# Performance work log

Hardware: AMD Instinct MI355X
Metric: run time of the kernel (lower is better)

The kernel has to match this reference:

```python
import jax, jax.numpy as jnp
import numpy as np
from jax import lax

BLANK = 27
NEG = -1e30  # safe -inf substitute (avoids NaN grads through logaddexp)


def _joint_log_probs(enc, dec, We, Wd, bf, Wp, bp):
    # Concat-then-Linear == sum of per-branch matmuls: [e;d] @ Wf = e@We + d@Wd.
    f = jnp.einsum('bte,eh->bth', enc, We)          # [B,T,H]
    g = jnp.einsum('bud,dh->buh', dec, Wd)          # [B,U1,H]
    h = jnp.tanh(f[:, :, None, :] + g[:, None, :, :] + bf)  # [B,T,U1,H]
    logits = jnp.einsum('btuh,hv->btuv', h, Wp) + bp         # [B,T,U1,V]
    return jax.nn.log_softmax(logits, axis=-1)


def _rnnt_loss_one(lp, tgt, t_len, u_len):
    # lp: [T,U1,V] log-probs, tgt: [U] int labels, t_len/u_len: scalars.
    T, U1, V = lp.shape
    blank_lp = lp[:, :, BLANK]                                   # [T,U1]
    lab_lp = jnp.take_along_axis(lp[:, :U1 - 1, :],
                                 tgt[None, :, None], axis=2)[..., 0]  # [T,U]

    # alpha[0,:] : only label emissions along u at t=0.
    alpha0 = jnp.concatenate([jnp.zeros((1,), lp.dtype),
                              jnp.cumsum(lab_lp[0])])            # [U1]

    def step(prev_alpha, inp):
        b_prev, lab_t = inp                       # [U1], [U]
        from_below = prev_alpha + b_prev          # blank move from t-1
        first = from_below[0]

        def inner(carry, x):
            fb, lab = x
            new = jnp.logaddexp(fb, carry + lab)  # blank-from-below vs label-from-left
            return new, new

        _, rest = lax.scan(inner, first, (from_below[1:], lab_t))
        alpha_t = jnp.concatenate([first[None], rest])
        return alpha_t, alpha_t

    _, alphas = lax.scan(step, alpha0, (blank_lp[:-1], lab_lp[1:]))
    alpha = jnp.concatenate([alpha0[None], alphas], axis=0)      # [T,U1]

    # Terminal: emit final blank at (t_len-1, u_len).
    return -(alpha[t_len - 1, u_len] + blank_lp[t_len - 1, u_len])


def setup_inputs() -> dict:
    key = jax.random.key(0)
    ks = jax.random.split(key, 10)
    B, T, U, E, D, H, V = 8, 400, 60, 256, 256, 512, 28
    enc_state = jax.random.normal(ks[0], (B, T, E), jnp.float32)
    dec_state = jax.random.normal(ks[1], (B, U + 1, D), jnp.float32)
    targets = jax.random.randint(ks[2], (B, U), 0, BLANK, jnp.int32)
    inputs_length = jax.random.randint(ks[3], (B,), 200, T + 1, jnp.int32)
    targets_length = jax.random.randint(ks[4], (B,), 30, U + 1, jnp.int32)
    s1 = 1.0 / np.sqrt(E + D)
    s2 = 1.0 / np.sqrt(H)
    We = jax.random.normal(ks[5], (E, H), jnp.float32) * s1
    Wd = jax.random.normal(ks[6], (D, H), jnp.float32) * s1
    bf = jax.random.normal(ks[7], (H,), jnp.float32) * s1
    Wp = jax.random.normal(ks[8], (H, V), jnp.float32) * s2
    bp = jax.random.normal(ks[9], (V,), jnp.float32) * s2
    return {"enc_state": enc_state, "dec_state": dec_state,
            "We": We, "Wd": Wd, "bf": bf, "Wp": Wp, "bp": bp,
            "targets": targets, "inputs_length": inputs_length,
            "targets_length": targets_length}


def reference(enc_state, dec_state, We, Wd, bf, Wp, bp,
              targets, inputs_length, targets_length):
    lp = _joint_log_probs(enc_state, dec_state, We, Wd, bf, Wp, bp)
    loss = jax.vmap(_rnnt_loss_one)(lp, targets, inputs_length, targets_length)
    return loss  # [B], reduction='none'
```

## Files before the change

### kernel.cpp

```cpp
#include <hip/hip_runtime.h>
#include <hip/hip_bf16.h>
#include <math.h>

#define NEGF (-1e30f)
#define LOG2E 1.4426950408889634f

typedef __attribute__((ext_vector_type(8))) short bf16x8;
typedef __attribute__((ext_vector_type(4))) float f32x4;

#define DROWS_PAD 480
#define DPITCH 64
#define D_TRIP 464
#define PF 16

__device__ __forceinline__ float tanh_fast(float x) {
    float e2 = __builtin_amdgcn_exp2f(x * 2.885390081777927f);
    return fmaf(-2.f, __builtin_amdgcn_rcpf(e2 + 1.f), 1.f);
}

__device__ __forceinline__ unsigned short f2bf(float x) {
    __hip_bfloat16 h = __float2bfloat16(x);
    return *reinterpret_cast<unsigned short*>(&h);
}

__device__ __forceinline__ float wave_shr1(float x) {
    int i = __builtin_bit_cast(int, x);
    int r = __builtin_amdgcn_update_dpp(0, i, 0x138, 0xf, 0xf, true);
    return __builtin_bit_cast(float, r);
}

__global__ __launch_bounds__(256) void k_pack(const float* __restrict__ We,
                                              const float* __restrict__ Wd,
                                              const float* __restrict__ Wp,
                                              unsigned short* __restrict__ WeFrag,
                                              unsigned short* __restrict__ WdFrag,
                                              unsigned short* __restrict__ BfragP) {
    int gid = blockIdx.x * 256 + threadIdx.x;
    if (gid < 32768) {
        const float* W = (gid < 16384) ? We : Wd;
        unsigned short* F = (gid < 16384) ? WeFrag : WdFrag;
        int s = gid & 16383;
        int lane = s & 63;
        int c = (s >> 6) & 7;
        int nt = s >> 9;
        int n = nt * 16 + (lane & 15);
        int kbase = c * 32 + ((lane >> 4) & 3) * 8;
        unsigned short* dst = F + (size_t)s * 8;
#pragma unroll
        for (int j = 0; j < 8; ++j) dst[j] = f2bf(W[(size_t)(kbase + j) * 512 + n]);
    } else if (gid < 34816) {
        int s = gid - 32768;
        int lane = s & 63;
        int half = (s >> 6) & 1;
        int c = s >> 7;
        int n = half * 16 + (lane & 15);
        int kbase = c * 32 + (lane >> 4) * 8;
        unsigned short* dst = BfragP + (size_t)s * 8;
#pragma unroll
        for (int j = 0; j < 8; ++j) {
            float v = (n < 28) ? Wp[(kbase + j) * 28 + n] : 0.f;
            dst[j] = f2bf(v);
        }
    }
}

__global__ __launch_bounds__(256) void k_gemm(const float* __restrict__ enc,
                                              const float* __restrict__ dec,
                                              const float* __restrict__ bfv,
                                              const unsigned short* __restrict__ WeFrag,
                                              const unsigned short* __restrict__ WdFrag,
                                              float* __restrict__ f,
                                              float* __restrict__ g) {
    const int wid = blockIdx.x * 4 + threadIdx.y;
    const int lane = threadIdx.x;
    const int m16 = lane & 15;
    const int quad = lane >> 4;

    const float* A; const unsigned short* WF; float* Out; int M, rt, ct; bool isg;
    if (wid < 1600) { A = enc; WF = WeFrag; Out = f; M = 3200; rt = wid >> 3; ct = wid & 7; isg = false; }
    else { int w2 = wid - 1600; A = dec; WF = WdFrag; Out = g; M = 488; rt = w2 >> 3; ct = w2 & 7; isg = true; }

    const int row = rt * 16 + m16;
    const float* arow = A + (size_t)min(row, M - 1) * 256 + quad * 8;

    f32x4 acc[4];
#pragma unroll
    for (int i = 0; i < 4; ++i) acc[i] = (f32x4){0.f, 0.f, 0.f, 0.f};

#pragma unroll
    for (int c = 0; c < 8; ++c) {
        float4 a0 = *(const float4*)(arow + c * 32);
        float4 a1 = *(const float4*)(arow + c * 32 + 4);
        union { unsigned short s[8]; bf16x8 v; } Af;
        Af.s[0] = f2bf(a0.x); Af.s[1] = f2bf(a0.y);
        Af.s[2] = f2bf(a0.z); Af.s[3] = f2bf(a0.w);
        Af.s[4] = f2bf(a1.x); Af.s[5] = f2bf(a1.y);
        Af.s[6] = f2bf(a1.z); Af.s[7] = f2bf(a1.w);
#pragma unroll
        for (int i = 0; i < 4; ++i) {
            int nt = ct * 4 + i;
            bf16x8 Bv = *(const bf16x8*)(WF + (size_t)((nt * 8 + c) * 64 + lane) * 8);
            acc[i] = __builtin_amdgcn_mfma_f32_16x16x32_bf16(Af.v, Bv, acc[i], 0, 0, 0);
        }
    }

#pragma unroll
    for (int i = 0; i < 4; ++i) {
        int n = ct * 64 + i * 16 + m16;
        float bv = isg ? bfv[n] : 0.f;
#pragma unroll
        for (int r = 0; r < 4; ++r) {
            int ro = rt * 16 + quad * 4 + r;
            if (ro < M) Out[(size_t)ro * 512 + n] = acc[i][r] + bv;
        }
    }
}

__global__ __launch_bounds__(256) void k_cells(const float* __restrict__ f,
                                               const float* __restrict__ g,
                                               const unsigned short* __restrict__ Bfrag,
                                               const float* __restrict__ bp,
                                               const int* __restrict__ targets,
                                               const int* __restrict__ ilen,
                                               float2* __restrict__ pairD) {
    const int b = blockIdx.z;
    const int tlen = ilen[b];
    const int t0 = blockIdx.x * 16;
    if (t0 >= tlen) return;
    const int wave = threadIdx.y;
    const int lane = threadIdx.x;
    const int u_raw = blockIdx.y * 4 + wave;
    const int u = min(u_raw, 60);
    const int tid = wave * 64 + lane;

    __shared__ float fs[16 * 516];

    {
        const float4* src = (const float4*)(f + (size_t)(b * 400 + t0) * 512);
#pragma unroll
        for (int i = 0; i < 8; ++i) {
            int idx = tid + i * 256;
            int row = idx >> 7;
            int c4 = idx & 127;
            float4 v = src[idx];
            *(float4*)&fs[row * 516 + c4 * 4] = v;
        }
    }
    __syncthreads();

    const int quad = lane >> 4;
    const int m16 = lane & 15;
    const float* gu = g + (size_t)(b * 61 + u) * 512 + quad * 8;
    const float* fsrow = fs + m16 * 516 + quad * 8;
    f32x4 acc0 = {0.f, 0.f, 0.f, 0.f};
    f32x4 acc1 = {0.f, 0.f, 0.f, 0.f};

#pragma unroll 4
    for (int c = 0; c < 16; ++c) {
        float4 fa = *(const float4*)(fsrow + c * 32);
        float4 fb = *(const float4*)(fsrow + c * 32 + 4);
        float4 ga = *(const float4*)(gu + c * 32);
        float4 gb = *(const float4*)(gu + c * 32 + 4);
        union { unsigned short s[8]; bf16x8 v; } A;
        A.s[0] = f2bf(tanh_fast(fa.x + ga.x));
        A.s[1] = f2bf(tanh_fast(fa.y + ga.y));
        A.s[2] = f2bf(tanh_fast(fa.z + ga.z));
        A.s[3] = f2bf(tanh_fast(fa.w + ga.w));
        A.s[4] = f2bf(tanh_fast(fb.x + gb.x));
        A.s[5] = f2bf(tanh_fast(fb.y + gb.y));
        A.s[6] = f2bf(tanh_fast(fb.z + gb.z));
        A.s[7] = f2bf(tanh_fast(fb.w + gb.w));
        bf16x8 B0 = *(const bf16x8*)(Bfrag + ((size_t)(c * 2 + 0) * 64 + lane) * 8);
        bf16x8 B1 = *(const bf16x8*)(Bfrag + ((size_t)(c * 2 + 1) * 64 + lane) * 8);
        acc0 = __builtin_amdgcn_mfma_f32_16x16x32_bf16(A.v, B0, acc0, 0, 0, 0);
        acc1 = __builtin_amdgcn_mfma_f32_16x16x32_bf16(A.v, B1, acc1, 0, 0, 0);
    }

    float bp0 = bp[m16];
    int n1 = 16 + m16;
    bool n1v = (n1 < 28);
    float bp1 = n1v ? bp[n1] : 0.f;
    int tv = targets[b * 60 + min(u, 59)];

    float res_blank[4], res_lab[4];
#pragma unroll
    for (int r = 0; r < 4; ++r) {
        float l0 = acc0[r] + bp0;
        float l1 = n1v ? (acc1[r] + bp1) : NEGF;
        float mx = fmaxf(l0, l1);
        mx = fmaxf(mx, __shfl_xor(mx, 1, 64));
        mx = fmaxf(mx, __shfl_xor(mx, 2, 64));
        mx = fmaxf(mx, __shfl_xor(mx, 4, 64));
        mx = fmaxf(mx, __shfl_xor(mx, 8, 64));
        float s = __builtin_amdgcn_exp2f((l0 - mx) * LOG2E) +
                  __builtin_amdgcn_exp2f((l1 - mx) * LOG2E);
        s += __shfl_xor(s, 1, 64);
        s += __shfl_xor(s, 2, 64);
        s += __shfl_xor(s, 4, 64);
        s += __shfl_xor(s, 8, 64);
        float lse = mx + __logf(s);
        int base = lane & 48;
        float labsrc = (tv < 16) ? l0 : l1;
        float labv = __shfl(labsrc, base | (tv & 15), 64);
        float blankv = __shfl(l1, base | 11, 64);
        res_blank[r] = blankv - lse;
        res_lab[r] = labv - lse;
    }

    if (m16 == 0 && u_raw <= 60) {
        float2* Pd = pairD + (size_t)b * (DROWS_PAD * DPITCH);
#pragma unroll
        for (int r = 0; r < 4; ++r) {
            int t = t0 + quad * 4 + r;
            if (t < tlen) {
                int d = t + u;
                float2 pr;
                pr.x = res_blank[r];
                pr.y = (u <= 59) ? res_lab[r] : NEGF;
                Pd[d * DPITCH + u] = pr;
            }
        }
    }
}

__global__ __launch_bounds__(64) void k_alpha(const float2* __restrict__ pairD,
                                              const int* __restrict__ ilen,
                                              const int* __restrict__ ulenp,
                                              float* __restrict__ out) {
    const int b = blockIdx.x;
    const int u = threadIdx.x;
    const float2* Pd = pairD + (size_t)b * (DROWS_PAD * DPITCH);
    const int tl = ilen[b];
    const int ul = ulenp[b];
    const int dstar = tl - 1 + ul;
    const bool uok = (u <= 60);
    const bool lok = (u >= 1 && u <= 60);

    float cur = (u == 0) ? 0.f : NEGF;
    float saved = NEGF;

    float2 pf[PF];
#pragma unroll
    for (int i = 0; i < PF; ++i) pf[i] = Pd[i * DPITCH + u];

    for (int d0 = 1; d0 <= D_TRIP; d0 += PF) {
#pragma unroll
        for (int i = 0; i < PF; ++i) {
            const int d = d0 + i;
            float2 v = pf[i];
            pf[i] = Pd[(d + PF - 1) * DPITCH + u];
            int t = d - u;
            float bv = (t >= 1 && t <= 399 && uok) ? v.x : NEGF;
            float lvn = wave_shr1(v.y);
            float lv = (lok && t >= 0 && t <= 399) ? lvn : NEGF;
            float up = wave_shr1(cur);
            float a = cur + bv;
            float c2 = up + lv;
            float mx = fmaxf(a, c2), mn = fminf(a, c2);
            float nv = mx + __logf(1.f + __builtin_amdgcn_exp2f((mn - mx) * LOG2E));
            bool valid = (t >= 0 && t <= 399 && uok);
            cur = valid ? nv : cur;
            saved = (d == dstar) ? cur : saved;
        }
    }
    if (u == ul) out[b] = -(saved + Pd[dstar * DPITCH + u].x);
}

extern "C" void kernel_launch(void* const* d_in, const int* in_sizes, int n_in,
                              void* d_out, int out_size, void* d_ws, size_t ws_size,
                              hipStream_t stream) {
    const float* enc = (const float*)d_in[0];
    const float* dec = (const float*)d_in[1];
    const float* We  = (const float*)d_in[2];
    const float* Wd  = (const float*)d_in[3];
    const float* bf  = (const float*)d_in[4];
    const float* Wp  = (const float*)d_in[5];
    const float* bp  = (const float*)d_in[6];
    const int* targets = (const int*)d_in[7];
    const int* ilen    = (const int*)d_in[8];
    const int* ulen    = (const int*)d_in[9];
    float* out = (float*)d_out;
    float* ws = (float*)d_ws;

    float* f     = ws;
    float* g     = ws + 1638400;
    unsigned short* BfragP = (unsigned short*)(ws + 1888256);
    unsigned short* WeFrag = (unsigned short*)(ws + 1896448);
    unsigned short* WdFrag = (unsigned short*)(ws + 1961984);
    float2* pairD = (float2*)(ws + 2027520);

    k_pack<<<136, 256, 0, stream>>>(We, Wd, Wp, WeFrag, WdFrag, BfragP);

    k_gemm<<<462, dim3(64, 4, 1), 0, stream>>>(enc, dec, bf, WeFrag, WdFrag, f, g);

    dim3 gridC(25, 16, 8);
    dim3 blockC(64, 4, 1);
    k_cells<<<gridC, blockC, 0, stream>>>(f, g, BfragP, bp, targets, ilen, pairD);

    k_alpha<<<8, 64, 0, stream>>>(pairD, ilen, ulen, out);
}
```

Before: 158.8 us.

## Fold tanh into sigmoid via weight rescaling, skip cells beyond target length, trim alpha loop

Rewrites tanh(x) as 1-2*sigmoid(2x) and folds the constants into the weights: f/g are prescaled by 2*log2e, Wp is multiplied by -2, and column sums of Wp plus bp become a new bias. The kernel then only needs exp2 plus a bit-trick reciprocal with one Newton step instead of the hardware rcp. k_cells also skips blocks whose u range lies past the target length, and k_alpha bounds its diagonal loop by the actual terminal diagonal instead of a fixed maximum. The aim is fewer ALU ops per joint cell and less wasted work, at the risk of lower reciprocal accuracy and bf16 rounding of the rescaled values.

```diff
diff --git a/kernel.cpp b/kernel.cpp
--- a/kernel.cpp
+++ b/kernel.cpp
@@ -4,19 +4,14 @@
 
 #define NEGF (-1e30f)
 #define LOG2E 1.4426950408889634f
+#define TSCALE 2.885390081777927f
 
 typedef __attribute__((ext_vector_type(8))) short bf16x8;
 typedef __attribute__((ext_vector_type(4))) float f32x4;
 
 #define DROWS_PAD 480
 #define DPITCH 64
-#define D_TRIP 464
 #define PF 16
-
-__device__ __forceinline__ float tanh_fast(float x) {
-    float e2 = __builtin_amdgcn_exp2f(x * 2.885390081777927f);
-    return fmaf(-2.f, __builtin_amdgcn_rcpf(e2 + 1.f), 1.f);
-}
 
 __device__ __forceinline__ unsigned short f2bf(float x) {
     __hip_bfloat16 h = __float2bfloat16(x);
@@ -29,12 +24,27 @@
     return __builtin_bit_cast(float, r);
 }
 
+__device__ __forceinline__ float4 rcp4_nr(float4 d) {
+    float4 y;
+    y.x = __builtin_bit_cast(float, 0x7EF311C3 - __builtin_bit_cast(int, d.x));
+    y.y = __builtin_bit_cast(float, 0x7EF311C3 - __builtin_bit_cast(int, d.y));
+    y.z = __builtin_bit_cast(float, 0x7EF311C3 - __builtin_bit_cast(int, d.z));
+    y.w = __builtin_bit_cast(float, 0x7EF311C3 - __builtin_bit_cast(int, d.w));
+    float4 t;
+    t.x = fmaf(-d.x, y.x, 2.f); t.y = fmaf(-d.y, y.y, 2.f);
+    t.z = fmaf(-d.z, y.z, 2.f); t.w = fmaf(-d.w, y.w, 2.f);
+    y.x *= t.x; y.y *= t.y; y.z *= t.z; y.w *= t.w;
+    return y;
+}
+
 __global__ __launch_bounds__(256) void k_pack(const float* __restrict__ We,
                                               const float* __restrict__ Wd,
                                               const float* __restrict__ Wp,
+                                              const float* __restrict__ bp,
                                               unsigned short* __restrict__ WeFrag,
                                               unsigned short* __restrict__ WdFrag,
-                                              unsigned short* __restrict__ BfragP) {
+                                              unsigned short* __restrict__ BfragP,
+                                              float* __restrict__ csbp) {
     int gid = blockIdx.x * 256 + threadIdx.x;
     if (gid < 32768) {
         const float* W = (gid < 16384) ? We : Wd;
@@ -58,9 +68,17 @@
         unsigned short* dst = BfragP + (size_t)s * 8;
 #pragma unroll
         for (int j = 0; j < 8; ++j) {
-            float v = (n < 28) ? Wp[(kbase + j) * 28 + n] : 0.f;
+            float v = (n < 28) ? (-2.f * Wp[(kbase + j) * 28 + n]) : 0.f;
             dst[j] = f2bf(v);
         }
+    } else if (gid < 34848) {
+        int v = gid - 34816;
+        float s = 0.f;
+        if (v < 28) {
+            for (int k = 0; k < 512; ++k) s += Wp[k * 28 + v];
+            s += bp[v];
+        }
+        csbp[v] = s;
     }
 }
 
@@ -111,7 +129,7 @@
 #pragma unroll
         for (int r = 0; r < 4; ++r) {
             int ro = rt * 16 + quad * 4 + r;
-            if (ro < M) Out[(size_t)ro * 512 + n] = acc[i][r] + bv;
+            if (ro < M) Out[(size_t)ro * 512 + n] = (acc[i][r] + bv) * TSCALE;
         }
     }
 }
@@ -119,14 +137,16 @@
 __global__ __launch_bounds__(256) void k_cells(const float* __restrict__ f,
                                                const float* __restrict__ g,
                                                const unsigned short* __restrict__ Bfrag,
-                                               const float* __restrict__ bp,
+                                               const float* __restrict__ csbp,
                                                const int* __restrict__ targets,
                                                const int* __restrict__ ilen,
+                                               const int* __restrict__ ulenp,
                                                float2* __restrict__ pairD) {
     const int b = blockIdx.z;
     const int tlen = ilen[b];
     const int t0 = blockIdx.x * 16;
     if (t0 >= tlen) return;
+    if ((int)blockIdx.y * 4 > ulenp[b]) return;
     const int wave = threadIdx.y;
     const int lane = threadIdx.x;
     const int u_raw = blockIdx.y * 4 + wave;
@@ -154,6 +174,7 @@
     const float* fsrow = fs + m16 * 516 + quad * 8;
     f32x4 acc0 = {0.f, 0.f, 0.f, 0.f};
     f32x4 acc1 = {0.f, 0.f, 0.f, 0.f};
+    const float4 one4 = make_float4(1.f, 1.f, 1.f, 1.f);
 
 #pragma unroll 4
     for (int c = 0; c < 16; ++c) {
@@ -161,32 +182,37 @@
         float4 fb = *(const float4*)(fsrow + c * 32 + 4);
         float4 ga = *(const float4*)(gu + c * 32);
         float4 gb = *(const float4*)(gu + c * 32 + 4);
+        float4 s0 = fa + ga;
+        float4 s1 = fb + gb;
+        float4 e0, e1;
+        e0.x = __builtin_amdgcn_exp2f(s0.x); e0.y = __builtin_amdgcn_exp2f(s0.y);
+        e0.z = __builtin_amdgcn_exp2f(s0.z); e0.w = __builtin_amdgcn_exp2f(s0.w);
+        e1.x = __builtin_amdgcn_exp2f(s1.x); e1.y = __builtin_amdgcn_exp2f(s1.y);
+        e1.z = __builtin_amdgcn_exp2f(s1.z); e1.w = __builtin_amdgcn_exp2f(s1.w);
+        float4 r0 = rcp4_nr(e0 + one4);
+        float4 r1 = rcp4_nr(e1 + one4);
         union { unsigned short s[8]; bf16x8 v; } A;
-        A.s[0] = f2bf(tanh_fast(fa.x + ga.x));
-        A.s[1] = f2bf(tanh_fast(fa.y + ga.y));
-        A.s[2] = f2bf(tanh_fast(fa.z + ga.z));
-        A.s[3] = f2bf(tanh_fast(fa.w + ga.w));
-        A.s[4] = f2bf(tanh_fast(fb.x + gb.x));
-        A.s[5] = f2bf(tanh_fast(fb.y + gb.y));
-        A.s[6] = f2bf(tanh_fast(fb.z + gb.z));
-        A.s[7] = f2bf(tanh_fast(fb.w + gb.w));
+        A.s[0] = f2bf(r0.x); A.s[1] = f2bf(r0.y);
+        A.s[2] = f2bf(r0.z); A.s[3] = f2bf(r0.w);
+        A.s[4] = f2bf(r1.x); A.s[5] = f2bf(r1.y);
+        A.s[6] = f2bf(r1.z); A.s[7] = f2bf(r1.w);
         bf16x8 B0 = *(const bf16x8*)(Bfrag + ((size_t)(c * 2 + 0) * 64 + lane) * 8);
         bf16x8 B1 = *(const bf16x8*)(Bfrag + ((size_t)(c * 2 + 1) * 64 + lane) * 8);
         acc0 = __builtin_amdgcn_mfma_f32_16x16x32_bf16(A.v, B0, acc0, 0, 0, 0);
         acc1 = __builtin_amdgcn_mfma_f32_16x16x32_bf16(A.v, B1, acc1, 0, 0, 0);
     }
 
-    float bp0 = bp[m16];
+    float cs0 = csbp[m16];
     int n1 = 16 + m16;
     bool n1v = (n1 < 28);
-    float bp1 = n1v ? bp[n1] : 0.f;
+    float cs1 = csbp[n1 & 31];
     int tv = targets[b * 60 + min(u, 59)];
 
     float res_blank[4], res_lab[4];
 #pragma unroll
     for (int r = 0; r < 4; ++r) {
-        float l0 = acc0[r] + bp0;
-        float l1 = n1v ? (acc1[r] + bp1) : NEGF;
+        float l0 = acc0[r] + cs0;
+        float l1 = n1v ? (acc1[r] + cs1) : NEGF;
         float mx = fmaxf(l0, l1);
         mx = fmaxf(mx, __shfl_xor(mx, 1, 64));
         mx = fmaxf(mx, __shfl_xor(mx, 2, 64));
@@ -233,6 +259,7 @@
     const int tl = ilen[b];
     const int ul = ulenp[b];
     const int dstar = tl - 1 + ul;
+    const int dmax = ((dstar + PF - 1) / PF) * PF;
     const bool uok = (u <= 60);
     const bool lok = (u >= 1 && u <= 60);
 
@@ -243,7 +270,7 @@
 #pragma unroll
     for (int i = 0; i < PF; ++i) pf[i] = Pd[i * DPITCH + u];
 
-    for (int d0 = 1; d0 <= D_TRIP; d0 += PF) {
+    for (int d0 = 1; d0 <= dmax; d0 += PF) {
 #pragma unroll
         for (int i = 0; i < PF; ++i) {
             const int d = d0 + i;
@@ -287,15 +314,16 @@
     unsigned short* BfragP = (unsigned short*)(ws + 1888256);
     unsigned short* WeFrag = (unsigned short*)(ws + 1896448);
     unsigned short* WdFrag = (unsigned short*)(ws + 1961984);
-    float2* pairD = (float2*)(ws + 2027520);
-
-    k_pack<<<136, 256, 0, stream>>>(We, Wd, Wp, WeFrag, WdFrag, BfragP);
+    float* csbp  = ws + 2027520;
+    float2* pairD = (float2*)(ws + 2027552);
+
+    k_pack<<<137, 256, 0, stream>>>(We, Wd, Wp, bp, WeFrag, WdFrag, BfragP, csbp);
 
     k_gemm<<<462, dim3(64, 4, 1), 0, stream>>>(enc, dec, bf, WeFrag, WdFrag, f, g);
 
     dim3 gridC(25, 16, 8);
     dim3 blockC(64, 4, 1);
-    k_cells<<<gridC, blockC, 0, stream>>>(f, g, BfragP, bp, targets, ilen, pairD);
+    k_cells<<<gridC, blockC, 0, stream>>>(f, g, BfragP, csbp, targets, ilen, ulen, pairD);
 
     k_alpha<<<8, 64, 0, stream>>>(pairD, ilen, ulen, out);
 }
```

Result: no change. 158.3 us (-0.3%).
